# Optimization experiments

Measured on AMD Instinct MI355X. Metric: run time of the kernel, lower is better.

Reference implementation:

```python
import jax, jax.numpy as jnp
import numpy as np

ALPHA, GAMMA = 0.25, 2.0
ACCEPT, REJECT = 0.5, 0.4
CLF_W, REG_W = 1.0, 50.0
SL1_R = 9.0  # reg_smooth_l1_loss_scaling_factor
EPS = 1e-4


def _calc_iou(a, b):
    # a: [A,4] anchors in yxyx ; b: [M,4] gt boxes in xyxy (as in original code)
    ay1, ax1, ay2, ax2 = a[:, 0], a[:, 1], a[:, 2], a[:, 3]
    bx1, by1, bx2, by2 = b[:, 0], b[:, 1], b[:, 2], b[:, 3]
    iw = jnp.clip(jnp.minimum(ax2[:, None], bx2) - jnp.maximum(ax1[:, None], bx1), 0.0)
    ih = jnp.clip(jnp.minimum(ay2[:, None], by2) - jnp.maximum(ay1[:, None], by1), 0.0)
    inter = iw * ih  # [A, M]
    aarea = ((ax2 - ax1) * (ay2 - ay1))[:, None]
    barea = (bx2 - bx1) * (by2 - by1)
    union = jnp.clip(aarea + barea - inter, 1e-8)
    return inter / union


def _single_image(clf, reg, ann, anchors, a_cx, a_cy, a_w, a_h):
    # clf: [A,C], reg: [A,4], ann: [M,5] (x1,y1,x2,y2,label; label=-1 => pad)
    clf = jnp.clip(clf, EPS, 1.0 - EPS)
    labels = ann[:, 4]
    valid = labels != -1.0  # [M]
    boxes = ann[:, :4]
    iou = _calc_iou(anchors, boxes)               # [A, M]
    iou = jnp.where(valid[None, :], iou, -1.0)    # invalid GT never matches
    iou_max = iou.max(axis=-1)                    # [A]
    iou_arg = iou.argmax(axis=-1)                 # [A]
    matched = iou_max > ACCEPT
    unmatched = iou_max < REJECT
    num_matched = matched.sum()
    # classification targets: -1 (ignore) by default, 0 for unmatched, one-hot for matched
    gt_lbl = labels[iou_arg].astype(jnp.int32) - 1  # [A]
    one_hot = jax.nn.one_hot(gt_lbl, clf.shape[-1], dtype=clf.dtype)
    tgt = jnp.where(matched[:, None], one_hot,
                    jnp.where(unmatched[:, None], 0.0, -1.0))
    pos = ALPHA * (1.0 - clf) ** GAMMA * (-jnp.log(clf))
    neg = (1.0 - ALPHA) * clf ** GAMMA * (-jnp.log(1.0 - clf))
    clf_losses = jnp.where(tgt == 1.0, pos, neg)
    clf_losses = jnp.where(tgt == -1.0, 0.0, clf_losses)
    clf_loss = clf_losses.sum() / jnp.maximum(1, num_matched).astype(clf.dtype)
    gb = boxes[iou_arg]  # [A,4] xyxy
    gw_raw = gb[:, 2] - gb[:, 0]
    gh_raw = gb[:, 3] - gb[:, 1]
    gcx = gb[:, 0] + 0.5 * gw_raw
    gcy = gb[:, 1] + 0.5 * gh_raw
    gw = jnp.clip(gw_raw, 1.0)
    gh = jnp.clip(gh_raw, 1.0)
    reg_t = jnp.stack(((gcy - a_cy) / a_h,
                       (gcx - a_cx) / a_w,
                       jnp.log(gh / a_h),
                       jnp.log(gw / a_w)), axis=-1)  # [A,4] (dy,dx,dh,dw)
    d = jnp.abs(SL1_R * (reg - reg_t))
    sl1 = jnp.where(d < 1.0, 0.5 * d * d, d - 0.5)
    sl1 = jnp.where(matched[:, None], sl1, 0.0)
    denom = jnp.maximum(1, 4 * num_matched).astype(clf.dtype)
    reg_loss = jnp.where(num_matched > 0, sl1.sum() / denom, 0.0)
    return clf_loss, reg_loss


def setup_inputs() -> dict:
    key = jax.random.key(0)
    ks = jax.random.split(key, 12)
    B, A, C, M = 8, 49104, 90, 32
    clf = jax.random.uniform(ks[0], (B, A, C), jnp.float32)
    reg = jax.random.normal(ks[1], (B, A, 4), jnp.float32)
    # anchors in yxyx, all with positive width/height
    y1 = jax.random.uniform(ks[2], (A,)) * 480.0
    x1 = jax.random.uniform(ks[3], (A,)) * 480.0
    ah = jax.random.uniform(ks[4], (A,)) * 120.0 + 8.0
    aw = jax.random.uniform(ks[5], (A,)) * 120.0 + 8.0
    anchors = jnp.stack([y1, x1, y1 + ah, x1 + aw], axis=-1)[None].astype(jnp.float32)
    # annotations: xyxy boxes + label in [1, C]; ~half padded with label -1
    bx1 = jax.random.uniform(ks[6], (B, M)) * 400.0
    by1 = jax.random.uniform(ks[7], (B, M)) * 400.0
    bw = jax.random.uniform(ks[8], (B, M)) * 100.0 + 20.0
    bh = jax.random.uniform(ks[9], (B, M)) * 100.0 + 20.0
    lbl = jax.random.randint(ks[10], (B, M), 1, C + 1).astype(jnp.float32)
    lbl = jnp.where(jax.random.uniform(ks[11], (B, M)) < 0.6, lbl, -1.0)
    ann = jnp.stack([bx1, by1, bx1 + bw, by1 + bh, lbl], axis=-1).astype(jnp.float32)
    return {"classifications": clf, "regressions": reg, "anchors": anchors, "annotations": ann}


def reference(classifications, regressions, anchors, annotations):
    anc = anchors.squeeze()  # [A,4] yxyx
    a_w = anc[:, 3] - anc[:, 1]
    a_h = anc[:, 2] - anc[:, 0]
    a_cx = anc[:, 1] + 0.5 * a_w
    a_cy = anc[:, 0] + 0.5 * a_h
    clf = jnp.clip(classifications, EPS, 1.0 - EPS)
    clf_l, reg_l = jax.vmap(_single_image, in_axes=(0, 0, 0, None, None, None, None, None))(
        clf, regressions, annotations, anc, a_cx, a_cy, a_w, a_h)
    return CLF_W * clf_l.mean(), REG_W * reg_l.mean()
```

## Files before the change

kernel.cpp:

```cpp
#include <hip/hip_runtime.h>


namespace {
constexpr int B_N = 8;
constexpr int A_N = 49104;
constexpr int C_N = 90;
constexpr int M_N = 32;
constexpr float EPSF   = 1e-4f;
constexpr float ACCEPT = 0.5f;
constexpr float REJECT = 0.4f;
constexpr float SL1R   = 9.0f;
constexpr float CLFW   = 1.0f;
constexpr float REGW   = 50.0f;

constexpr int APB     = 256;
constexpr int NBX     = (A_N + APB - 1) / APB;

__device__ __forceinline__ float clampx(float x) {
    return __builtin_amdgcn_fmed3f(x, EPSF, 1.0f - EPSF);
}
}

__global__ void fused_kernel(const float* __restrict__ anchors,
                             const float* __restrict__ reg,
                             const float* __restrict__ ann,
                             const float* __restrict__ clf,
                             float4* __restrict__ part)
{
    __shared__ float sann[M_N * 5];
    __shared__ int   sstate[APB];
    __shared__ float sred[4][3];

    const int b   = blockIdx.y;
    const int a0  = blockIdx.x * APB;
    const int tid = threadIdx.x;
    if (tid < M_N * 5) sann[tid] = ann[b * M_N * 5 + tid];
    __syncthreads();

    float cnt  = 0.0f;
    float rsum = 0.0f;
    int   s    = -2;
    const int i = a0 + tid;

    if (i < A_N) {
        const float4 av = ((const float4*)anchors)[i];
        const float ay1 = av.x, ax1 = av.y, ay2 = av.z, ax2 = av.w;
        const float aw = ax2 - ax1, ah = ay2 - ay1;
        const float aarea = aw * ah;

        float best = -3.4e38f;
        int   arg  = 0;
        #pragma unroll 8
        for (int j = 0; j < M_N; ++j) {
            const float bx1 = sann[j*5+0], by1 = sann[j*5+1];
            const float bx2 = sann[j*5+2], by2 = sann[j*5+3];
            const float lb  = sann[j*5+4];
            float iw = fminf(ax2, bx2) - fmaxf(ax1, bx1); iw = fmaxf(iw, 0.0f);
            float ih = fminf(ay2, by2) - fmaxf(ay1, by1); ih = fmaxf(ih, 0.0f);
            const float inter = iw * ih;
            const float barea = (bx2 - bx1) * (by2 - by1);
            const float uni   = fmaxf(aarea + barea - inter, 1e-8f);
            float iou = inter / uni;
            if (lb == -1.0f) iou = -1.0f;
            if (iou > best) { best = iou; arg = j; }
        }

        const bool matched   = best > ACCEPT;
        const bool unmatched = best < REJECT;

        if (matched) {
            s   = (int)sann[arg*5+4] - 1;
            cnt = 1.0f;
            const float bx1 = sann[arg*5+0], by1 = sann[arg*5+1];
            const float bx2 = sann[arg*5+2], by2 = sann[arg*5+3];
            const float gwr = bx2 - bx1, ghr = by2 - by1;
            const float gcx = bx1 + 0.5f * gwr, gcy = by1 + 0.5f * ghr;
            const float gw  = fmaxf(gwr, 1.0f), gh = fmaxf(ghr, 1.0f);
            const float acx = ax1 + 0.5f * aw, acy = ay1 + 0.5f * ah;
            const float t0 = (gcy - acy) / ah;
            const float t1 = (gcx - acx) / aw;
            const float t2 = __logf(gh / ah);
            const float t3 = __logf(gw / aw);
            const float4 rv = ((const float4*)reg)[b * A_N + i];
            float d;
            d = fabsf(SL1R * (rv.x - t0)); rsum += (d < 1.0f) ? 0.5f*d*d : d - 0.5f;
            d = fabsf(SL1R * (rv.y - t1)); rsum += (d < 1.0f) ? 0.5f*d*d : d - 0.5f;
            d = fabsf(SL1R * (rv.z - t2)); rsum += (d < 1.0f) ? 0.5f*d*d : d - 0.5f;
            d = fabsf(SL1R * (rv.w - t3)); rsum += (d < 1.0f) ? 0.5f*d*d : d - 0.5f;
        } else {
            s = unmatched ? -1 : -2;
        }
    }
    sstate[tid] = s;
    __syncthreads();

    const int nA  = min(APB, A_N - a0);
    const int nF4 = nA * C_N / 4;
    const float4* __restrict__ p =
        (const float4*)(clf + ((size_t)b * A_N + a0) * C_N);

    float csum = 0.0f;

    auto term = [&](float x, int st, int c) -> float {
        const bool ispos = (st == c);
        x = clampx(x);
        const float y  = ispos ? x : 1.0f - x;
        float al = ispos ? -0.25f : -0.75f;
        al = (st == -2) ? 0.0f : al;
        const float o = 1.0f - y;
        return al * o * o * __logf(y);
    };

    for (int f = tid; f < nF4; f += 256) {
        const float4 v = p[f];
        const int idx = 4 * f;
        const int a   = (int)((unsigned)idx / 90u);
        const int c0  = idx - 90 * a;
        const bool strad = (c0 == 88);
        const int s0 = sstate[a];
        const int s1 = strad ? sstate[a + 1] : s0;
        const int c2 = strad ? 0 : c0 + 2;
        const int c3 = strad ? 1 : c0 + 3;
        csum += term(v.x, s0, c0);
        csum += term(v.y, s0, c0 + 1);
        csum += term(v.z, s1, c2);
        csum += term(v.w, s1, c3);
    }

    #pragma unroll
    for (int off = 32; off > 0; off >>= 1) {
        cnt  += __shfl_down(cnt,  off);
        rsum += __shfl_down(rsum, off);
        csum += __shfl_down(csum, off);
    }
    const int wid = tid >> 6;
    if ((tid & 63) == 0) {
        sred[wid][0] = cnt; sred[wid][1] = rsum; sred[wid][2] = csum;
    }
    __syncthreads();
    if (tid == 0) {
        float c = 0.f, r = 0.f, k = 0.f;
        #pragma unroll
        for (int w = 0; w < 4; ++w) { c += sred[w][0]; r += sred[w][1]; k += sred[w][2]; }
        part[b * NBX + blockIdx.x] = make_float4(c, r, k, 0.0f);
    }
}

__global__ void finalize_kernel(const float4* __restrict__ part,
                                float*        __restrict__ out)
{
    __shared__ float s_cnt[B_N], s_rsum[B_N], s_csum[B_N];
    const int tid = threadIdx.x;
    const int b   = tid >> 5;
    const int j   = tid & 31;

    float cnt = 0.f, rsum = 0.f, csum = 0.f;
    #pragma unroll
    for (int k = 0; k < NBX / 32; ++k) {
        const float4 m = part[b * NBX + j + 32 * k];
        cnt += m.x; rsum += m.y; csum += m.z;
    }
    #pragma unroll
    for (int off = 16; off > 0; off >>= 1) {
        cnt  += __shfl_down(cnt,  off, 32);
        rsum += __shfl_down(rsum, off, 32);
        csum += __shfl_down(csum, off, 32);
    }
    if (j == 0) { s_cnt[b] = cnt; s_rsum[b] = rsum; s_csum[b] = csum; }
    __syncthreads();
    if (tid == 0) {
        float cl = 0.0f, rl = 0.0f;
        #pragma unroll
        for (int bb = 0; bb < B_N; ++bb) {
            const float n = s_cnt[bb];
            cl += s_csum[bb] / fmaxf(1.0f, n);
            if (n > 0.0f) rl += s_rsum[bb] / (4.0f * n);
        }
        out[0] = CLFW * (cl / (float)B_N);
        out[1] = REGW * (rl / (float)B_N);
    }
}

extern "C" void kernel_launch(void* const* d_in, const int* in_sizes, int n_in,
                              void* d_out, int out_size, void* d_ws, size_t ws_size,
                              hipStream_t stream) {
    const float* clf     = (const float*)d_in[0];
    const float* reg     = (const float*)d_in[1];
    const float* anchors = (const float*)d_in[2];
    const float* ann     = (const float*)d_in[3];
    float*  out  = (float*)d_out;
    float4* part = (float4*)d_ws;

    {
        dim3 grid(NBX, B_N);
        fused_kernel<<<grid, 256, 0, stream>>>(anchors, reg, ann, clf, part);
    }
    finalize_kernel<<<1, 256, 0, stream>>>(part, out);
}
```

Measured before the change: 218.3 us.

## Compute uniform negative focal term over all elements, correct matched and ignored anchors sparsely

The main loop now applies the negative focal term x^2*log2(1-x) to every classification element, with no per-element state lookup, division or branching, and is unrolled four loads deep. Matched anchors (pos minus neg at one class) and ignored anchors (subtract the whole row) are collected in shared lists via shared atomics and corrected in a second sparse pass. The finalize kernel scales by -0.75*ln2 and adds the correction. This trades a small amount of redundant work and extra scattered rereads of clf for a much simpler, memory-bound streaming loop; float summation order changes.

```diff
diff --git a/kernel.cpp b/kernel.cpp
--- a/kernel.cpp
+++ b/kernel.cpp
@@ -12,12 +12,22 @@
 constexpr float SL1R   = 9.0f;
 constexpr float CLFW   = 1.0f;
 constexpr float REGW   = 50.0f;
-
-constexpr int APB     = 256;
-constexpr int NBX     = (A_N + APB - 1) / APB;
+constexpr float LN2    = 0.69314718055994530942f;
+
+constexpr int APB = 256;
+constexpr int NBX = (A_N + APB - 1) / APB;
 
 __device__ __forceinline__ float clampx(float x) {
     return __builtin_amdgcn_fmed3f(x, EPSF, 1.0f - EPSF);
+}
+__device__ __forceinline__ float neg_term(float x) {
+    x = clampx(x);
+    return 0.75f * x * x * (-__logf(1.0f - x));
+}
+__device__ __forceinline__ float pos_term(float x) {
+    x = clampx(x);
+    float o = 1.0f - x;
+    return 0.25f * o * o * (-__logf(x));
 }
 }
 
@@ -28,18 +38,21 @@
                              float4* __restrict__ part)
 {
     __shared__ float sann[M_N * 5];
-    __shared__ int   sstate[APB];
-    __shared__ float sred[4][3];
+    __shared__ int   s_match[APB];
+    __shared__ int   s_ign[APB];
+    __shared__ int   s_nm, s_ni;
+    __shared__ float sred[4][4];
 
     const int b   = blockIdx.y;
     const int a0  = blockIdx.x * APB;
     const int tid = threadIdx.x;
     if (tid < M_N * 5) sann[tid] = ann[b * M_N * 5 + tid];
+    if (tid == 0) { s_nm = 0; s_ni = 0; }
     __syncthreads();
 
     float cnt  = 0.0f;
     float rsum = 0.0f;
-    int   s    = -2;
+    float corr = 0.0f;
     const int i = a0 + tid;
 
     if (i < A_N) {
@@ -69,8 +82,10 @@
         const bool unmatched = best < REJECT;
 
         if (matched) {
-            s   = (int)sann[arg*5+4] - 1;
+            const int s = (int)sann[arg*5+4] - 1;
             cnt = 1.0f;
+            const int slot = atomicAdd(&s_nm, 1);
+            s_match[slot] = (tid << 8) | s;
             const float bx1 = sann[arg*5+0], by1 = sann[arg*5+1];
             const float bx2 = sann[arg*5+2], by2 = sann[arg*5+3];
             const float gwr = bx2 - bx1, ghr = by2 - by1;
@@ -87,11 +102,11 @@
             d = fabsf(SL1R * (rv.y - t1)); rsum += (d < 1.0f) ? 0.5f*d*d : d - 0.5f;
             d = fabsf(SL1R * (rv.z - t2)); rsum += (d < 1.0f) ? 0.5f*d*d : d - 0.5f;
             d = fabsf(SL1R * (rv.w - t3)); rsum += (d < 1.0f) ? 0.5f*d*d : d - 0.5f;
-        } else {
-            s = unmatched ? -1 : -2;
-        }
-    }
-    sstate[tid] = s;
+        } else if (!unmatched) {
+            const int slot = atomicAdd(&s_ni, 1);
+            s_ign[slot] = tid;
+        }
+    }
     __syncthreads();
 
     const int nA  = min(APB, A_N - a0);
@@ -99,81 +114,102 @@
     const float4* __restrict__ p =
         (const float4*)(clf + ((size_t)b * A_N + a0) * C_N);
 
-    float csum = 0.0f;
-
-    auto term = [&](float x, int st, int c) -> float {
-        const bool ispos = (st == c);
-        x = clampx(x);
-        const float y  = ispos ? x : 1.0f - x;
-        float al = ispos ? -0.25f : -0.75f;
-        al = (st == -2) ? 0.0f : al;
-        const float o = 1.0f - y;
-        return al * o * o * __logf(y);
+    float S = 0.0f;
+
+    auto w4 = [](float4 v) -> float {
+        float s = 0.0f;
+        const float x0 = clampx(v.x), x1 = clampx(v.y);
+        const float x2 = clampx(v.z), x3 = clampx(v.w);
+        s = fmaf(x0 * x0, __log2f(1.0f - x0), s);
+        s = fmaf(x1 * x1, __log2f(1.0f - x1), s);
+        s = fmaf(x2 * x2, __log2f(1.0f - x2), s);
+        s = fmaf(x3 * x3, __log2f(1.0f - x3), s);
+        return s;
     };
 
-    for (int f = tid; f < nF4; f += 256) {
-        const float4 v = p[f];
-        const int idx = 4 * f;
-        const int a   = (int)((unsigned)idx / 90u);
-        const int c0  = idx - 90 * a;
-        const bool strad = (c0 == 88);
-        const int s0 = sstate[a];
-        const int s1 = strad ? sstate[a + 1] : s0;
-        const int c2 = strad ? 0 : c0 + 2;
-        const int c3 = strad ? 1 : c0 + 3;
-        csum += term(v.x, s0, c0);
-        csum += term(v.y, s0, c0 + 1);
-        csum += term(v.z, s1, c2);
-        csum += term(v.w, s1, c3);
+    int f = tid;
+    #pragma unroll 1
+    for (; f + 768 < nF4; f += 1024) {
+        const float4 v0 = p[f];
+        const float4 v1 = p[f + 256];
+        const float4 v2 = p[f + 512];
+        const float4 v3 = p[f + 768];
+        S += w4(v0) + w4(v1) + w4(v2) + w4(v3);
+    }
+    for (; f < nF4; f += 256) S += w4(p[f]);
+
+    const int nm = s_nm, ni = s_ni;
+    for (int k = tid; k < nm; k += 256) {
+        const int packed = s_match[k];
+        const int a  = packed >> 8;
+        const int sc = packed & 0xFF;
+        const float x = clf[((size_t)b * A_N + a0 + a) * C_N + sc];
+        corr += pos_term(x) - neg_term(x);
+    }
+    const int wid  = tid >> 6;
+    const int lane = tid & 63;
+    for (int e = wid; e < ni; e += 4) {
+        const int a = s_ign[e];
+        const float2* __restrict__ r2 =
+            (const float2*)(clf + ((size_t)b * A_N + a0 + a) * C_N);
+        if (lane < 45) {
+            const float2 u = r2[lane];
+            corr -= neg_term(u.x) + neg_term(u.y);
+        }
     }
 
     #pragma unroll
     for (int off = 32; off > 0; off >>= 1) {
         cnt  += __shfl_down(cnt,  off);
         rsum += __shfl_down(rsum, off);
-        csum += __shfl_down(csum, off);
-    }
-    const int wid = tid >> 6;
-    if ((tid & 63) == 0) {
-        sred[wid][0] = cnt; sred[wid][1] = rsum; sred[wid][2] = csum;
+        S    += __shfl_down(S,    off);
+        corr += __shfl_down(corr, off);
+    }
+    if (lane == 0) {
+        sred[wid][0] = cnt; sred[wid][1] = rsum;
+        sred[wid][2] = S;   sred[wid][3] = corr;
     }
     __syncthreads();
     if (tid == 0) {
-        float c = 0.f, r = 0.f, k = 0.f;
+        float c = 0.f, r = 0.f, ss = 0.f, k = 0.f;
         #pragma unroll
-        for (int w = 0; w < 4; ++w) { c += sred[w][0]; r += sred[w][1]; k += sred[w][2]; }
-        part[b * NBX + blockIdx.x] = make_float4(c, r, k, 0.0f);
+        for (int w = 0; w < 4; ++w) {
+            c += sred[w][0]; r += sred[w][1]; ss += sred[w][2]; k += sred[w][3];
+        }
+        part[b * NBX + blockIdx.x] = make_float4(c, r, ss, k);
     }
 }
 
 __global__ void finalize_kernel(const float4* __restrict__ part,
                                 float*        __restrict__ out)
 {
-    __shared__ float s_cnt[B_N], s_rsum[B_N], s_csum[B_N];
+    __shared__ float s_cnt[B_N], s_rsum[B_N], s_S[B_N], s_corr[B_N];
     const int tid = threadIdx.x;
     const int b   = tid >> 5;
     const int j   = tid & 31;
 
-    float cnt = 0.f, rsum = 0.f, csum = 0.f;
+    float cnt = 0.f, rsum = 0.f, S = 0.f, corr = 0.f;
     #pragma unroll
     for (int k = 0; k < NBX / 32; ++k) {
         const float4 m = part[b * NBX + j + 32 * k];
-        cnt += m.x; rsum += m.y; csum += m.z;
+        cnt += m.x; rsum += m.y; S += m.z; corr += m.w;
     }
     #pragma unroll
     for (int off = 16; off > 0; off >>= 1) {
         cnt  += __shfl_down(cnt,  off, 32);
         rsum += __shfl_down(rsum, off, 32);
-        csum += __shfl_down(csum, off, 32);
-    }
-    if (j == 0) { s_cnt[b] = cnt; s_rsum[b] = rsum; s_csum[b] = csum; }
+        S    += __shfl_down(S,    off, 32);
+        corr += __shfl_down(corr, off, 32);
+    }
+    if (j == 0) { s_cnt[b] = cnt; s_rsum[b] = rsum; s_S[b] = S; s_corr[b] = corr; }
     __syncthreads();
     if (tid == 0) {
         float cl = 0.0f, rl = 0.0f;
         #pragma unroll
         for (int bb = 0; bb < B_N; ++bb) {
             const float n = s_cnt[bb];
-            cl += s_csum[bb] / fmaxf(1.0f, n);
+            const float clf_total = -0.75f * LN2 * s_S[bb] + s_corr[bb];
+            cl += clf_total / fmaxf(1.0f, n);
             if (n > 0.0f) rl += s_rsum[bb] / (4.0f * n);
         }
         out[0] = CLFW * (cl / (float)B_N);
```

New measurement: 215.2 us. About the same (-1.4%).
